# Kernel tuning notes

Hardware: AMD Instinct MI355X
Metric: run time of the kernel (lower is better)

## Reference

```python
import jax, jax.numpy as jnp
import numpy as np
from jax import lax

B, T, V = 128, 100, 100000
ED, MD, H = 300, 50, 512   # embed_dim, mask_dim, l_hidden_size
HH = H // 2                # per-direction GRU hidden
C1 = 0.1
C2 = 0.1


def _reverse_valid(x, lens):
    # reverse the valid prefix of each sequence (emulates packed-sequence reverse dir)
    t = jnp.arange(x.shape[1])[None, :]
    idx = jnp.where(t < lens[:, None], lens[:, None] - 1 - t, t)
    return jnp.take_along_axis(x, idx[:, :, None], axis=1)


def _gru_dir(x, valid, lens, wih, whh, bih, bhh, reverse):
    # x: [B,T,Din], valid: [B,T] bool. PyTorch GRU cell math, packed-seq semantics:
    # state frozen and output zeroed at padded steps.
    if reverse:
        x = _reverse_valid(x, lens)
    h0 = jnp.zeros((x.shape[0], whh.shape[1]), x.dtype)
    def step(h, inp):
        xt, mt = inp
        gi = xt @ wih.T + bih
        gh = h @ whh.T + bhh
        ir, iz, inn = jnp.split(gi, 3, axis=-1)
        hr, hz, hn = jnp.split(gh, 3, axis=-1)
        r = jax.nn.sigmoid(ir + hr)
        z = jax.nn.sigmoid(iz + hz)
        n = jnp.tanh(inn + r * hn)
        hnew = (1.0 - z) * n + z * h
        hnew = jnp.where(mt[:, None], hnew, h)
        return hnew, jnp.where(mt[:, None], hnew, 0.0)
    _, out = lax.scan(step, h0, (x.transpose(1, 0, 2), valid.T))
    out = out.transpose(1, 0, 2)
    if reverse:
        out = _reverse_valid(out, lens)
    return out


def _crf_marginals(feats, L, trans):
    # linear-chain CRF forward-backward marginals, 2 latent states; feats [T,2], valid length L
    Tm = feats.shape[0]
    def fstep(alpha, inp):
        ft, t = inp
        new = jax.nn.logsumexp(alpha[:, None] + trans, axis=0) + ft
        a = jnp.where(t < L, new, alpha)
        return a, a
    a0 = feats[0]
    _, rest = lax.scan(fstep, a0, (feats[1:], jnp.arange(1, Tm)))
    alphas = jnp.concatenate([a0[None], rest], axis=0)
    logZ = jax.nn.logsumexp(alphas[L - 1])
    def bstep(beta, inp):
        fn, t = inp
        cand = jax.nn.logsumexp(trans + (fn + beta)[None, :], axis=1)
        b = jnp.where(t >= L - 1, jnp.zeros_like(cand), cand)
        return b, b
    _, brev = lax.scan(bstep, jnp.zeros((2,), feats.dtype), (feats[1:][::-1], jnp.arange(Tm - 2, -1, -1)))
    betas = jnp.concatenate([brev[::-1], jnp.zeros((1, 2), feats.dtype)], axis=0)
    marg = jnp.exp(alphas + betas - logZ)
    return jnp.where(jnp.arange(Tm)[:, None] < L, marg, 0.0)


def setup_inputs():
    key = jax.random.key(0)
    ks = jax.random.split(key, 30)
    s = 0.08
    inp = {}
    inp["sents"] = jax.random.randint(ks[0], (B, T), 0, V, dtype=jnp.int32)
    lens = jnp.sort(jax.random.randint(ks[1], (B,), 5, T + 1, dtype=jnp.int32))[::-1]
    inp["lens"] = lens
    t = jnp.arange(T)[None, :]
    start = (lens // 3)[:, None]
    inp["masks"] = ((t >= start) & (t < start + 3)).astype(jnp.int32)
    inp["labels"] = jax.random.randint(ks[2], (B,), 0, 3, dtype=jnp.int32)
    inp["word_emb"] = jax.random.normal(ks[3], (V, ED)) * s
    inp["mask_emb"] = jax.random.normal(ks[4], (2, MD)) * s
    i = 5
    for l, din in ((0, ED + MD), (1, H)):
        for d in ("f", "b"):
            inp[f"gru{l}{d}_wih"] = jax.random.normal(ks[i], (3 * HH, din)) * s; i += 1
            inp[f"gru{l}{d}_whh"] = jax.random.normal(ks[i], (3 * HH, HH)) * s; i += 1
            inp[f"gru{l}{d}_bih"] = jnp.zeros((3 * HH,))
            inp[f"gru{l}{d}_bhh"] = jnp.zeros((3 * HH,))
    inp["conv_w"] = jax.random.normal(ks[i], (H, H, 3)) * s; i += 1
    inp["conv_b"] = jnp.zeros((H,))
    inp["tri_w"] = jax.random.normal(ks[i], (2, 2 * H)) * s; i += 1
    inp["tri_b"] = jnp.zeros((2,))
    inp["trans"] = jax.random.normal(ks[i], (2, 2)) * s; i += 1
    inp["lab_w"] = jax.random.normal(ks[i], (3, H)) * s; i += 1
    inp["lab_b"] = jnp.zeros((3,))
    return inp


def _forward(sents, masks, labels, lens, word_emb, mask_emb, gru_params, conv_w, conv_b, tri_w, tri_b, trans, lab_w, lab_b):
    x = jnp.concatenate([word_emb[sents], mask_emb[masks]], axis=-1)  # SimpleCat
    valid = jnp.arange(T)[None, :] < lens[:, None]
    for layer in range(2):  # 2-layer bidirectional GRU
        pf, pb = gru_params[2 * layer], gru_params[2 * layer + 1]
        f = _gru_dir(x, valid, lens, *pf, False)
        b = _gru_dir(x, valid, lens, *pb, True)
        x = jnp.concatenate([f, b], axis=-1)
    context = jax.nn.relu(
        lax.conv_general_dilated(x, conv_w.transpose(2, 1, 0), (1,), [(1, 1)],
                                 dimension_numbers=("NWC", "WIO", "NWC")) + conv_b)
    mf = masks.astype(context.dtype)
    avg = jnp.einsum("bt,bth->bh", mf, context) / mf.sum(1, keepdims=True)  # target avg emb
    ctx1 = jnp.concatenate([context, jnp.broadcast_to(avg[:, None, :], context.shape)], axis=-1)
    tri = ctx1 @ tri_w.T + tri_b  # [B,T,2]
    marg = jax.vmap(_crf_marginals, in_axes=(0, 0, None))(tri, lens, trans)
    sp = marg[:, :, 1]  # select polarity, zeroed beyond each sent_len
    sent_v = jnp.einsum("bt,bth->bh", sp, context)
    gamma = jnp.clip(sp.sum(1) / 2.0, 1e-4, 1e5)
    scores = (sent_v / gamma[:, None]) @ lab_w.T + lab_b
    logp = jax.nn.log_softmax(scores, axis=-1)
    cls_loss = -jnp.mean(jnp.take_along_axis(logp, labels[:, None], axis=1))  # NLLLoss
    s_norm = jnp.mean(sp.sum(1))  # mean L1 norm of nonneg marginals
    pena = jax.nn.relu(trans[1, 0] - trans[0, 0]) + jax.nn.relu(trans[0, 1] - trans[1, 1])
    return jnp.stack([cls_loss, C1 * pena + C2 * s_norm])


def reference(sents, masks, labels, lens, word_emb, mask_emb, gru0f_wih, gru0f_whh, gru0f_bih, gru0f_bhh, gru0b_wih, gru0b_whh, gru0b_bih, gru0b_bhh, gru1f_wih, gru1f_whh, gru1f_bih, gru1f_bhh, gru1b_wih, gru1b_whh, gru1b_bih, gru1b_bhh, conv_w, conv_b, tri_w, tri_b, trans, lab_w, lab_b):
    gp = ((gru0f_wih, gru0f_whh, gru0f_bih, gru0f_bhh),
          (gru0b_wih, gru0b_whh, gru0b_bih, gru0b_bhh),
          (gru1f_wih, gru1f_whh, gru1f_bih, gru1f_bhh),
          (gru1b_wih, gru1b_whh, gru1b_bih, gru1b_bhh))
    return _forward(sents, masks, labels, lens, word_emb, mask_emb, gp, conv_w, conv_b, tri_w, tri_b, trans, lab_w, lab_b)
```

## Files before the change

### kernel.cpp

```cpp
#include <hip/hip_runtime.h>
#include <hip/hip_bf16.h>
#include <stdint.h>


#define TT 100
#define BB 128

typedef short s16;
typedef unsigned int u32;
typedef __attribute__((ext_vector_type(8))) short s16x8;
typedef __attribute__((ext_vector_type(4))) float f32x4;
typedef __attribute__((ext_vector_type(2))) float f32x2;

__device__ __forceinline__ float bf2f(s16 s) {
  return __uint_as_float(((unsigned)(unsigned short)s) << 16);
}
__device__ __forceinline__ s16 f2bf(float f) {
  __hip_bfloat16 h = __float2bfloat16(f);
  return *(s16*)&h;
}
__device__ __forceinline__ float sigf(float x) { return 1.f / (1.f + __expf(-x)); }
__device__ __forceinline__ float tanhfast(float x) { return 2.f / (1.f + __expf(-2.f * x)) - 1.f; }
__device__ __forceinline__ float lse2(float a, float b) {
  float m = fmaxf(a, b);
  return m + logf(expf(a - m) + expf(b - m));
}


__global__ void k_cvtpad(const float* __restrict__ src, s16* __restrict__ dst) {
  int idx = blockIdx.x * 256 + threadIdx.x;
  if (idx >= 768 * 352) return;
  int n = idx / 352, k = idx % 352;
  dst[idx] = (k < 350) ? f2bf(src[n * 350 + k]) : (s16)0;
}

__global__ void k_cvt(const float* __restrict__ src, s16* __restrict__ dst, int n) {
  int idx = blockIdx.x * 256 + threadIdx.x;
  if (idx < n) dst[idx] = f2bf(src[idx]);
}

__global__ void k_wfrag(const float* __restrict__ whh, s16* __restrict__ wf) {
  int tid = blockIdx.x * 256 + threadIdx.x;
  if (tid >= 196608) return;
  int w = tid / 24576, rem = tid % 24576;
  int f = rem / 512, rem2 = rem % 512;
  int l = rem2 / 8, i = rem2 % 8;
  int nt = f / 8, kt = f % 8;
  int col = 96 * w + 16 * nt + (l & 15);
  int k = 32 * kt + 8 * (l >> 4) + i;
  wf[tid] = f2bf(whh[col * 256 + k]);
}

__global__ void k_w2(const float* __restrict__ cw, s16* __restrict__ w2) {
  int idx = blockIdx.x * 256 + threadIdx.x;
  if (idx >= 786432) return;
  int o = idx / 1536, c = idx % 1536;
  int w = c / 512, i = c % 512;
  w2[idx] = f2bf(cw[o * 1536 + i * 3 + w]);
}

__global__ void k_embed(const int* __restrict__ sents, const int* __restrict__ masks,
                        const float* __restrict__ wemb, const float* __restrict__ memb,
                        s16* __restrict__ x0) {
  int idx = blockIdx.x * 256 + threadIdx.x;
  if (idx >= BB * TT * 352) return;
  int c = idx % 352, bt = idx / 352;
  float v;
  if (c < 300)      v = wemb[(size_t)sents[bt] * 300 + c];
  else if (c < 350) v = memb[masks[bt] * 50 + (c - 300)];
  else              v = 0.f;
  x0[idx] = f2bf(v);
}

__global__ void k_zero16(uint4* __restrict__ p, int n16) {
  int idx = blockIdx.x * 256 + threadIdx.x;
  if (idx < n16) p[idx] = make_uint4(0u, 0u, 0u, 0u);
}

__global__ __launch_bounds__(256) void k_gemm(const s16* __restrict__ A, const s16* __restrict__ Bm,
                                              s16* __restrict__ C, int K, int ldA, int ldB, int ldC,
                                              const float* __restrict__ bias, int relu) {
  __shared__ s16 As[128 * 32];
  __shared__ s16 Bs[128 * 32];
  const int t = threadIdx.x, w = t >> 6, l = t & 63;
  const size_t m0 = (size_t)blockIdx.x * 128, n0 = (size_t)blockIdx.y * 128;
  f32x4 zero = {0.f, 0.f, 0.f, 0.f};
  f32x4 acc[4][4];
#pragma unroll
  for (int i = 0; i < 4; ++i)
#pragma unroll
    for (int j = 0; j < 4; ++j) acc[i][j] = zero;

  for (int kb = 0; kb < K; kb += 32) {
    __syncthreads();
    {
      const s16* gA = A + (m0 + (t >> 1)) * (size_t)ldA + kb + 16 * (t & 1);
      *(s16x8*)&As[(t >> 1) * 32 + 16 * (t & 1)]     = *(const s16x8*)gA;
      *(s16x8*)&As[(t >> 1) * 32 + 16 * (t & 1) + 8] = *(const s16x8*)(gA + 8);
      const s16* gB = Bm + (n0 + (t >> 1)) * (size_t)ldB + kb + 16 * (t & 1);
      *(s16x8*)&Bs[(t >> 1) * 32 + 16 * (t & 1)]     = *(const s16x8*)gB;
      *(s16x8*)&Bs[(t >> 1) * 32 + 16 * (t & 1) + 8] = *(const s16x8*)(gB + 8);
    }
    __syncthreads();
    s16x8 a[4], b[4];
#pragma unroll
    for (int i = 0; i < 4; ++i)
      a[i] = *(const s16x8*)&As[(64 * (w >> 1) + 16 * i + (l & 15)) * 32 + 8 * (l >> 4)];
#pragma unroll
    for (int j = 0; j < 4; ++j)
      b[j] = *(const s16x8*)&Bs[(64 * (w & 1) + 16 * j + (l & 15)) * 32 + 8 * (l >> 4)];
#pragma unroll
    for (int i = 0; i < 4; ++i)
#pragma unroll
      for (int j = 0; j < 4; ++j)
        acc[i][j] = __builtin_amdgcn_mfma_f32_16x16x32_bf16(a[i], b[j], acc[i][j], 0, 0, 0);
  }
#pragma unroll
  for (int i = 0; i < 4; ++i)
#pragma unroll
    for (int j = 0; j < 4; ++j)
#pragma unroll
      for (int r = 0; r < 4; ++r) {
        size_t row = m0 + 64 * (w >> 1) + 16 * i + 4 * (l >> 4) + r;
        size_t col = n0 + 64 * (w & 1) + 16 * j + (l & 15);
        float v = acc[i][j][r];
        if (bias) v += bias[col];
        if (relu) v = fmaxf(v, 0.f);
        C[row * (size_t)ldC + col] = f2bf(v);
      }
}

__global__ __launch_bounds__(512, 2) void k_gru(
    const s16* __restrict__ gi_f, const s16* __restrict__ gi_b,
    const s16* __restrict__ wf_f, const s16* __restrict__ wf_b,
    const float* __restrict__ bhh_f, const float* __restrict__ bhh_b,
    const int* __restrict__ lens, s16* __restrict__ out) {
  const int g = blockIdx.x;
  const int dir = blockIdx.y;
  const int tid = threadIdx.x, wid = tid >> 6, l = tid & 63;
  const s16* gi = dir ? gi_b : gi_f;
  const s16* wf = dir ? wf_b : wf_f;
  const float* bhh = dir ? bhh_b : bhh_f;
  const int col_off = dir ? 256 : 0;
  const int b0 = g * 8;

  __shared__ __align__(16) float gh2[16 * 772];
  __shared__ __align__(16) s16 hb[16 * 264];
  __shared__ float s_bhh[768];
  __shared__ int s_len[8];

  s16x8 wv[48];
#pragma unroll
  for (int f = 0; f < 48; ++f)
    wv[f] = *(const s16x8*)&wf[((size_t)(wid * 48 + f)) * 512 + l * 8];

  for (int i = tid; i < 16 * 264; i += 512) hb[i] = 0;
  for (int i = tid; i < 768; i += 512) s_bhh[i] = bhh[i];
  if (tid < 8) s_len[tid] = lens[b0 + tid];
  __syncthreads();

  const int smax = s_len[0];

  const int j0 = (tid & 127) * 2;
  const int r0 = tid >> 7;
  const int len0 = s_len[r0];
  const int len1 = s_len[r0 + 4];
  const float bhr0 = s_bhh[j0],       bhr1 = s_bhh[j0 + 1];
  const float bhz0 = s_bhh[256 + j0], bhz1 = s_bhh[257 + j0];
  const float bhn0 = s_bhh[512 + j0], bhn1 = s_bhh[513 + j0];
  float hp00 = 0.f, hp01 = 0.f, hp10 = 0.f, hp11 = 0.f;

  for (int s = 0; s < smax; ++s) {
    u32 q00 = 0, q01 = 0, q02 = 0, q10 = 0, q11 = 0, q12 = 0;
    int p0 = 0, p1 = 0;
    if (s < len0) {
      p0 = dir ? (len0 - 1 - s) : s;
      const s16* gp = gi + ((size_t)(b0 + r0) * TT + p0) * 768 + j0;
      q00 = *(const u32*)gp; q01 = *(const u32*)(gp + 256); q02 = *(const u32*)(gp + 512);
    }
    if (s < len1) {
      p1 = dir ? (len1 - 1 - s) : s;
      const s16* gp = gi + ((size_t)(b0 + r0 + 4) * TT + p1) * 768 + j0;
      q10 = *(const u32*)gp; q11 = *(const u32*)(gp + 256); q12 = *(const u32*)(gp + 512);
    }

    f32x4 zero = {0.f, 0.f, 0.f, 0.f};
    f32x4 acc[6];
#pragma unroll
    for (int nt = 0; nt < 6; ++nt) acc[nt] = zero;
#pragma unroll
    for (int kt = 0; kt < 8; ++kt) {
      s16x8 a = *(const s16x8*)&hb[(l & 15) * 264 + 32 * kt + 8 * (l >> 4)];
#pragma unroll
      for (int nt = 0; nt < 6; ++nt)
        acc[nt] = __builtin_amdgcn_mfma_f32_16x16x32_bf16(a, wv[nt * 8 + kt], acc[nt], 0, 0, 0);
    }
#pragma unroll
    for (int nt = 0; nt < 6; ++nt) {
      int col = 96 * wid + 16 * nt + (l & 15);
#pragma unroll
      for (int r = 0; r < 4; ++r)
        gh2[(4 * (l >> 4) + r) * 772 + col] = acc[nt][r];
    }
    __syncthreads();

    if (s < len0) {
      f32x2 gr = *(const f32x2*)&gh2[r0 * 772 + j0];
      f32x2 gz = *(const f32x2*)&gh2[r0 * 772 + 256 + j0];
      f32x2 gn = *(const f32x2*)&gh2[r0 * 772 + 512 + j0];
      float rr0 = sigf(bf2f((s16)(q00 & 0xffff)) + gr[0] + bhr0);
      float rr1 = sigf(bf2f((s16)(q00 >> 16))    + gr[1] + bhr1);
      float zz0 = sigf(bf2f((s16)(q01 & 0xffff)) + gz[0] + bhz0);
      float zz1 = sigf(bf2f((s16)(q01 >> 16))    + gz[1] + bhz1);
      float nn0 = tanhfast(bf2f((s16)(q02 & 0xffff)) + rr0 * (gn[0] + bhn0));
      float nn1 = tanhfast(bf2f((s16)(q02 >> 16))    + rr1 * (gn[1] + bhn1));
      hp00 = (1.f - zz0) * nn0 + zz0 * hp00;
      hp01 = (1.f - zz1) * nn1 + zz1 * hp01;
      u32 pk = (u32)(unsigned short)f2bf(hp00) | ((u32)(unsigned short)f2bf(hp01) << 16);
      *(u32*)&hb[r0 * 264 + j0] = pk;
      *(u32*)&out[((size_t)(b0 + r0) * TT + p0) * 512 + col_off + j0] = pk;
    }
    if (s < len1) {
      int row = r0 + 4;
      f32x2 gr = *(const f32x2*)&gh2[row * 772 + j0];
      f32x2 gz = *(const f32x2*)&gh2[row * 772 + 256 + j0];
      f32x2 gn = *(const f32x2*)&gh2[row * 772 + 512 + j0];
      float rr0 = sigf(bf2f((s16)(q10 & 0xffff)) + gr[0] + bhr0);
      float rr1 = sigf(bf2f((s16)(q10 >> 16))    + gr[1] + bhr1);
      float zz0 = sigf(bf2f((s16)(q11 & 0xffff)) + gz[0] + bhz0);
      float zz1 = sigf(bf2f((s16)(q11 >> 16))    + gz[1] + bhz1);
      float nn0 = tanhfast(bf2f((s16)(q12 & 0xffff)) + rr0 * (gn[0] + bhn0));
      float nn1 = tanhfast(bf2f((s16)(q12 >> 16))    + rr1 * (gn[1] + bhn1));
      hp10 = (1.f - zz0) * nn0 + zz0 * hp10;
      hp11 = (1.f - zz1) * nn1 + zz1 * hp11;
      u32 pk = (u32)(unsigned short)f2bf(hp10) | ((u32)(unsigned short)f2bf(hp11) << 16);
      *(u32*)&hb[row * 264 + j0] = pk;
      *(u32*)&out[((size_t)(b0 + row) * TT + p1) * 512 + col_off + j0] = pk;
    }
    __syncthreads();
  }
}

__global__ void k_im2col(const s16* __restrict__ x2, s16* __restrict__ A2) {
  int idx = blockIdx.x * 256 + threadIdx.x;
  if (idx >= 2457600) return;
  size_t e = (size_t)idx * 8;
  int bt = (int)(e / 1536), c = (int)(e % 1536);
  int w = c / 512, i = c % 512;
  int b = bt / TT, t = bt % TT;
  int ts = t + w - 1;
  s16x8 v;
  if (ts >= 0 && ts < TT) v = *(const s16x8*)&x2[(size_t)(b * TT + ts) * 512 + i];
  else { s16x8 z = {0,0,0,0,0,0,0,0}; v = z; }
  *(s16x8*)&A2[e] = v;
}

__global__ void k_avg(const s16* __restrict__ ctx, const int* __restrict__ masks,
                      float* __restrict__ avg) {
  int b = blockIdx.x, t = threadIdx.x;
  float a0 = 0, a1 = 0, ms = 0;
  for (int tt = 0; tt < TT; ++tt) {
    float mf = (float)masks[b * TT + tt];
    ms += mf;
    if (mf != 0.f) {
      a0 += mf * bf2f(ctx[(size_t)(b * TT + tt) * 512 + t]);
      a1 += mf * bf2f(ctx[(size_t)(b * TT + tt) * 512 + 256 + t]);
    }
  }
  avg[b * 512 + t] = a0 / ms;
  avg[b * 512 + 256 + t] = a1 / ms;
}

__global__ void k_tri(const s16* __restrict__ ctx, const float* __restrict__ avg,
                      const float* __restrict__ triw, const float* __restrict__ trib,
                      float* __restrict__ tri) {
  int gw = (blockIdx.x * 256 + threadIdx.x) >> 6;
  int l = threadIdx.x & 63;
  if (gw >= BB * TT) return;
  int b = gw / TT;
  float a0 = 0, a1 = 0;
  for (int it = 0; it < 16; ++it) {
    int k = l + 64 * it;
    float v = (k < 512) ? bf2f(ctx[(size_t)gw * 512 + k]) : avg[b * 512 + k - 512];
    a0 += v * triw[k];
    a1 += v * triw[1024 + k];
  }
  for (int off = 32; off; off >>= 1) {
    a0 += __shfl_down(a0, off, 64);
    a1 += __shfl_down(a1, off, 64);
  }
  if (l == 0) {
    tri[gw * 2]     = a0 + trib[0];
    tri[gw * 2 + 1] = a1 + trib[1];
  }
}

__global__ void k_crf(const float* __restrict__ tri, const int* __restrict__ lens,
                      const float* __restrict__ trans, float* __restrict__ alphas,
                      float* __restrict__ sp, float* __restrict__ sp_sum) {
  int b = threadIdx.x;
  int L = lens[b];
  float t00 = trans[0], t01 = trans[1], t10 = trans[2], t11 = trans[3];
  const float* f = tri + b * 2 * TT;
  float* al = alphas + b * 2 * TT;
  float a0 = f[0], a1 = f[1];
  al[0] = a0; al[1] = a1;
  for (int t = 1; t < TT; ++t) {
    if (t < L) {
      float n0 = lse2(a0 + t00, a1 + t10) + f[2 * t];
      float n1 = lse2(a0 + t01, a1 + t11) + f[2 * t + 1];
      a0 = n0; a1 = n1;
    }
    al[2 * t] = a0; al[2 * t + 1] = a1;
  }
  float logZ = lse2(a0, a1);
  float b0 = 0.f, b1 = 0.f, ssum = 0.f;
  {
    float v = (TT - 1 < L) ? expf(al[2 * (TT - 1) + 1] - logZ) : 0.f;
    sp[b * TT + TT - 1] = v; ssum += v;
  }
  for (int t = TT - 2; t >= 0; --t) {
    float fn0 = f[2 * (t + 1)], fn1 = f[2 * (t + 1) + 1];
    float c0 = lse2(t00 + fn0 + b0, t01 + fn1 + b1);
    float c1 = lse2(t10 + fn0 + b0, t11 + fn1 + b1);
    if (t >= L - 1) { b0 = 0.f; b1 = 0.f; } else { b0 = c0; b1 = c1; }
    float v = (t < L) ? expf(al[2 * t + 1] + b1 - logZ) : 0.f;
    sp[b * TT + t] = v; ssum += v;
  }
  sp_sum[b] = ssum;
}

__global__ void k_sentv(const s16* __restrict__ ctx, const float* __restrict__ sp,
                        float* __restrict__ sv) {
  int b = blockIdx.x, t = threadIdx.x;
  float a0 = 0, a1 = 0;
  for (int tt = 0; tt < TT; ++tt) {
    float w = sp[b * TT + tt];
    if (w != 0.f) {
      a0 += w * bf2f(ctx[(size_t)(b * TT + tt) * 512 + t]);
      a1 += w * bf2f(ctx[(size_t)(b * TT + tt) * 512 + 256 + t]);
    }
  }
  sv[b * 512 + t] = a0;
  sv[b * 512 + 256 + t] = a1;
}

__global__ void k_final(const float* __restrict__ sv, const float* __restrict__ sp_sum,
                        const int* __restrict__ labels, const float* __restrict__ labw,
                        const float* __restrict__ labb, const float* __restrict__ trans,
                        float* __restrict__ out) {
  __shared__ float red[128];
  int b = threadIdx.x;
  float g = sp_sum[b] * 0.5f;
  g = fminf(fmaxf(g, 1e-4f), 1e5f);
  float s[3];
  for (int c = 0; c < 3; ++c) {
    float a = 0.f;
    for (int h = 0; h < 512; ++h) a += sv[b * 512 + h] * labw[c * 512 + h];
    s[c] = a / g + labb[c];
  }
  float m = fmaxf(s[0], fmaxf(s[1], s[2]));
  float lse = m + logf(expf(s[0] - m) + expf(s[1] - m) + expf(s[2] - m));
  red[b] = -(s[labels[b]] - lse);
  __syncthreads();
  if (b == 0) {
    float acc = 0.f, sn = 0.f;
    for (int i = 0; i < 128; ++i) { acc += red[i]; sn += sp_sum[i]; }
    float pena = fmaxf(trans[2] - trans[0], 0.f) + fmaxf(trans[1] - trans[3], 0.f);
    out[0] = acc / 128.f;
    out[1] = 0.1f * pena + 0.1f * (sn / 128.f);
  }
}

extern "C" void kernel_launch(void* const* d_in, const int* in_sizes, int n_in,
                              void* d_out, int out_size, void* d_ws, size_t ws_size,
                              hipStream_t stream) {
  const int*   sents  = (const int*)d_in[0];
  const int*   lens   = (const int*)d_in[1];
  const int*   masks  = (const int*)d_in[2];
  const int*   labels = (const int*)d_in[3];
  const float* wemb   = (const float*)d_in[4];
  const float* memb   = (const float*)d_in[5];
  const float* wih0f = (const float*)d_in[6],  *whh0f = (const float*)d_in[7];
  const float* bih0f = (const float*)d_in[8],  *bhh0f = (const float*)d_in[9];
  const float* wih0b = (const float*)d_in[10], *whh0b = (const float*)d_in[11];
  const float* bih0b = (const float*)d_in[12], *bhh0b = (const float*)d_in[13];
  const float* wih1f = (const float*)d_in[14], *whh1f = (const float*)d_in[15];
  const float* bih1f = (const float*)d_in[16], *bhh1f = (const float*)d_in[17];
  const float* wih1b = (const float*)d_in[18], *whh1b = (const float*)d_in[19];
  const float* bih1b = (const float*)d_in[20], *bhh1b = (const float*)d_in[21];
  const float* convw = (const float*)d_in[22], *convb = (const float*)d_in[23];
  const float* triw  = (const float*)d_in[24], *trib  = (const float*)d_in[25];
  const float* trans = (const float*)d_in[26];
  const float* labw  = (const float*)d_in[27], *labb  = (const float*)d_in[28];
  float* out = (float*)d_out;
  char* ws = (char*)d_ws;

  s16* x0    = (s16*)(ws + 0);
  s16* cwih0f = (s16*)(ws + 9011200);
  s16* cwih0b = (s16*)(ws + 9551872);
  s16* cwih1f = (s16*)(ws + 10092544);
  s16* cwih1b = (s16*)(ws + 10878976);
  s16* wf0f  = (s16*)(ws + 11665408);
  s16* wf0b  = (s16*)(ws + 12058624);
  s16* wf1f  = (s16*)(ws + 12451840);
  s16* wf1b  = (s16*)(ws + 12845056);
  s16* w2    = (s16*)(ws + 13238272);
  s16* giF   = (s16*)(ws + 14811136);
  s16* giB   = (s16*)(ws + 34471936);
  s16* x1    = (s16*)(ws + 54132736);
  s16* x2    = (s16*)(ws + 67239936);
  s16* A2    = giF;
  s16* ctx   = x1;
  float* avg   = (float*)(ws + 80347136);
  float* tri   = (float*)(ws + 80609280);
  float* alphas= (float*)(ws + 80711680);
  float* sp    = (float*)(ws + 80814080);
  float* spsum = (float*)(ws + 80865280);
  float* sentv = (float*)(ws + 80865792);

  k_cvtpad<<<1056, 256, 0, stream>>>(wih0f, cwih0f);
  k_cvtpad<<<1056, 256, 0, stream>>>(wih0b, cwih0b);
  k_cvt<<<1536, 256, 0, stream>>>(wih1f, cwih1f, 393216);
  k_cvt<<<1536, 256, 0, stream>>>(wih1b, cwih1b, 393216);
  k_wfrag<<<768, 256, 0, stream>>>(whh0f, wf0f);
  k_wfrag<<<768, 256, 0, stream>>>(whh0b, wf0b);
  k_wfrag<<<768, 256, 0, stream>>>(whh1f, wf1f);
  k_wfrag<<<768, 256, 0, stream>>>(whh1b, wf1b);
  k_w2<<<3072, 256, 0, stream>>>(convw, w2);
  k_embed<<<17600, 256, 0, stream>>>(sents, masks, wemb, memb, x0);
  k_zero16<<<3200, 256, 0, stream>>>((uint4*)x1, 819200);
  k_zero16<<<3200, 256, 0, stream>>>((uint4*)x2, 819200);

  k_gemm<<<dim3(100, 6), 256, 0, stream>>>(x0, cwih0f, giF, 352, 352, 352, 768, bih0f, 0);
  k_gemm<<<dim3(100, 6), 256, 0, stream>>>(x0, cwih0b, giB, 352, 352, 352, 768, bih0b, 0);
  k_gru<<<dim3(16, 2), 512, 0, stream>>>(giF, giB, wf0f, wf0b, bhh0f, bhh0b, lens, x1);

  k_gemm<<<dim3(100, 6), 256, 0, stream>>>(x1, cwih1f, giF, 512, 512, 512, 768, bih1f, 0);
  k_gemm<<<dim3(100, 6), 256, 0, stream>>>(x1, cwih1b, giB, 512, 512, 512, 768, bih1b, 0);
  k_gru<<<dim3(16, 2), 512, 0, stream>>>(giF, giB, wf1f, wf1b, bhh1f, bhh1b, lens, x2);

  k_im2col<<<9600, 256, 0, stream>>>(x2, A2);
  k_gemm<<<dim3(100, 4), 256, 0, stream>>>(A2, w2, ctx, 1536, 1536, 1536, 512, convb, 1);
  k_avg<<<128, 256, 0, stream>>>(ctx, masks, avg);
  k_tri<<<3200, 256, 0, stream>>>(ctx, avg, triw, trib, tri);
  k_crf<<<1, 128, 0, stream>>>(tri, lens, trans, alphas, sp, spsum);
  k_sentv<<<128, 256, 0, stream>>>(ctx, sp, sentv);
  k_final<<<1, 128, 0, stream>>>(sentv, spsum, labels, labw, labb, trans, out);
}
```

Before: 1.143 ms.

## Split GRU across more blocks, prefetch gate inputs, fold bias, fuse prep kernels

The GRU recurrence now gives each block 4 batch rows instead of 8, doubling the block count so the sequential loop spreads across more CUs and each thread handles half the elementwise gate work. Next-step input-gate values are loaded one iteration ahead so the global-load latency overlaps the MFMA work. The hidden bias is used as the initial MFMA accumulator, which removes the shared-memory bias table. The twelve weight-conversion, embedding and zeroing launches are merged into one grid-stride kernel, and the zeroing of x1 is dropped. In exchange, MFMA tiles still cover 16 rows, so more of each tile computes on padding rows.

After: 1.010 ms. 1.13x faster.

```diff
diff --git a/kernel.cpp b/kernel.cpp
--- a/kernel.cpp
+++ b/kernel.cpp
@@ -26,55 +26,57 @@
   return m + logf(expf(a - m) + expf(b - m));
 }
 
-
-__global__ void k_cvtpad(const float* __restrict__ src, s16* __restrict__ dst) {
-  int idx = blockIdx.x * 256 + threadIdx.x;
-  if (idx >= 768 * 352) return;
-  int n = idx / 352, k = idx % 352;
-  dst[idx] = (k < 350) ? f2bf(src[n * 350 + k]) : (s16)0;
-}
-
-__global__ void k_cvt(const float* __restrict__ src, s16* __restrict__ dst, int n) {
-  int idx = blockIdx.x * 256 + threadIdx.x;
-  if (idx < n) dst[idx] = f2bf(src[idx]);
-}
-
-__global__ void k_wfrag(const float* __restrict__ whh, s16* __restrict__ wf) {
-  int tid = blockIdx.x * 256 + threadIdx.x;
-  if (tid >= 196608) return;
-  int w = tid / 24576, rem = tid % 24576;
-  int f = rem / 512, rem2 = rem % 512;
-  int l = rem2 / 8, i = rem2 % 8;
-  int nt = f / 8, kt = f % 8;
-  int col = 96 * w + 16 * nt + (l & 15);
-  int k = 32 * kt + 8 * (l >> 4) + i;
-  wf[tid] = f2bf(whh[col * 256 + k]);
-}
-
-__global__ void k_w2(const float* __restrict__ cw, s16* __restrict__ w2) {
-  int idx = blockIdx.x * 256 + threadIdx.x;
-  if (idx >= 786432) return;
-  int o = idx / 1536, c = idx % 1536;
-  int w = c / 512, i = c % 512;
-  w2[idx] = f2bf(cw[o * 1536 + i * 3 + w]);
-}
-
-__global__ void k_embed(const int* __restrict__ sents, const int* __restrict__ masks,
-                        const float* __restrict__ wemb, const float* __restrict__ memb,
-                        s16* __restrict__ x0) {
-  int idx = blockIdx.x * 256 + threadIdx.x;
-  if (idx >= BB * TT * 352) return;
-  int c = idx % 352, bt = idx / 352;
-  float v;
-  if (c < 300)      v = wemb[(size_t)sents[bt] * 300 + c];
-  else if (c < 350) v = memb[masks[bt] * 50 + (c - 300)];
-  else              v = 0.f;
-  x0[idx] = f2bf(v);
-}
-
-__global__ void k_zero16(uint4* __restrict__ p, int n16) {
-  int idx = blockIdx.x * 256 + threadIdx.x;
-  if (idx < n16) p[idx] = make_uint4(0u, 0u, 0u, 0u);
+__global__ void k_prep(const float* __restrict__ wih0f, const float* __restrict__ wih0b,
+                       const float* __restrict__ wih1f, const float* __restrict__ wih1b,
+                       const float* __restrict__ whh0f, const float* __restrict__ whh0b,
+                       const float* __restrict__ whh1f, const float* __restrict__ whh1b,
+                       const float* __restrict__ convw,
+                       const int* __restrict__ sents, const int* __restrict__ masks,
+                       const float* __restrict__ wemb, const float* __restrict__ memb,
+                       s16* __restrict__ cwih0f, s16* __restrict__ cwih0b,
+                       s16* __restrict__ cwih1f, s16* __restrict__ cwih1b,
+                       s16* __restrict__ wf0f, s16* __restrict__ wf0b,
+                       s16* __restrict__ wf1f, s16* __restrict__ wf1b,
+                       s16* __restrict__ w2, s16* __restrict__ x0,
+                       uint4* __restrict__ x2z) {
+  const int stride = gridDim.x * 256;
+  const int base = blockIdx.x * 256 + threadIdx.x;
+
+  for (int idx = base; idx < 768 * 352; idx += stride) {
+    int n = idx / 352, k = idx % 352;
+    cwih0f[idx] = (k < 350) ? f2bf(wih0f[n * 350 + k]) : (s16)0;
+    cwih0b[idx] = (k < 350) ? f2bf(wih0b[n * 350 + k]) : (s16)0;
+  }
+  for (int idx = base; idx < 393216; idx += stride) {
+    cwih1f[idx] = f2bf(wih1f[idx]);
+    cwih1b[idx] = f2bf(wih1b[idx]);
+  }
+  for (int idx = base; idx < 196608; idx += stride) {
+    int w = idx / 24576, rem = idx % 24576;
+    int f = rem / 512, rem2 = rem % 512;
+    int l = rem2 / 8, i = rem2 % 8;
+    int nt = f / 8, kt = f % 8;
+    int src = (96 * w + 16 * nt + (l & 15)) * 256 + 32 * kt + 8 * (l >> 4) + i;
+    wf0f[idx] = f2bf(whh0f[src]);
+    wf0b[idx] = f2bf(whh0b[src]);
+    wf1f[idx] = f2bf(whh1f[src]);
+    wf1b[idx] = f2bf(whh1b[src]);
+  }
+  for (int idx = base; idx < 786432; idx += stride) {
+    int o = idx / 1536, c = idx % 1536;
+    int w = c / 512, i = c % 512;
+    w2[idx] = f2bf(convw[o * 1536 + i * 3 + w]);
+  }
+  for (int idx = base; idx < BB * TT * 352; idx += stride) {
+    int c = idx % 352, bt = idx / 352;
+    float v;
+    if (c < 300)      v = wemb[(size_t)sents[bt] * 300 + c];
+    else if (c < 350) v = memb[masks[bt] * 50 + (c - 300)];
+    else              v = 0.f;
+    x0[idx] = f2bf(v);
+  }
+  for (int idx = base; idx < 819200; idx += stride)
+    x2z[idx] = make_uint4(0u, 0u, 0u, 0u);
 }
 
 __global__ __launch_bounds__(256) void k_gemm(const s16* __restrict__ A, const s16* __restrict__ Bm,
@@ -142,52 +144,52 @@
   const s16* wf = dir ? wf_b : wf_f;
   const float* bhh = dir ? bhh_b : bhh_f;
   const int col_off = dir ? 256 : 0;
-  const int b0 = g * 8;
+  const int b0 = g * 4;
 
   __shared__ __align__(16) float gh2[16 * 772];
   __shared__ __align__(16) s16 hb[16 * 264];
-  __shared__ float s_bhh[768];
-  __shared__ int s_len[8];
+  __shared__ int s_len[4];
 
   s16x8 wv[48];
 #pragma unroll
   for (int f = 0; f < 48; ++f)
     wv[f] = *(const s16x8*)&wf[((size_t)(wid * 48 + f)) * 512 + l * 8];
+  float bv[6];
+#pragma unroll
+  for (int nt = 0; nt < 6; ++nt) bv[nt] = bhh[96 * wid + 16 * nt + (l & 15)];
 
   for (int i = tid; i < 16 * 264; i += 512) hb[i] = 0;
-  for (int i = tid; i < 768; i += 512) s_bhh[i] = bhh[i];
-  if (tid < 8) s_len[tid] = lens[b0 + tid];
+  if (tid < 4) s_len[tid] = lens[b0 + tid];
   __syncthreads();
 
   const int smax = s_len[0];
-
+  const int row = tid >> 7;
   const int j0 = (tid & 127) * 2;
-  const int r0 = tid >> 7;
-  const int len0 = s_len[r0];
-  const int len1 = s_len[r0 + 4];
-  const float bhr0 = s_bhh[j0],       bhr1 = s_bhh[j0 + 1];
-  const float bhz0 = s_bhh[256 + j0], bhz1 = s_bhh[257 + j0];
-  const float bhn0 = s_bhh[512 + j0], bhn1 = s_bhh[513 + j0];
-  float hp00 = 0.f, hp01 = 0.f, hp10 = 0.f, hp11 = 0.f;
+  const int len = s_len[row];
+  const s16* gbase = gi + (size_t)(b0 + row) * TT * 768 + j0;
+  s16* obase = out + (size_t)(b0 + row) * TT * 512 + col_off + j0;
+  float hp0 = 0.f, hp1 = 0.f;
+
+  u32 qa0, qa1, qa2;
+  int pa;
+  {
+    pa = dir ? (len - 1) : 0;
+    const s16* gp = gbase + (size_t)pa * 768;
+    qa0 = *(const u32*)gp; qa1 = *(const u32*)(gp + 256); qa2 = *(const u32*)(gp + 512);
+  }
 
   for (int s = 0; s < smax; ++s) {
-    u32 q00 = 0, q01 = 0, q02 = 0, q10 = 0, q11 = 0, q12 = 0;
-    int p0 = 0, p1 = 0;
-    if (s < len0) {
-      p0 = dir ? (len0 - 1 - s) : s;
-      const s16* gp = gi + ((size_t)(b0 + r0) * TT + p0) * 768 + j0;
-      q00 = *(const u32*)gp; q01 = *(const u32*)(gp + 256); q02 = *(const u32*)(gp + 512);
-    }
-    if (s < len1) {
-      p1 = dir ? (len1 - 1 - s) : s;
-      const s16* gp = gi + ((size_t)(b0 + r0 + 4) * TT + p1) * 768 + j0;
-      q10 = *(const u32*)gp; q11 = *(const u32*)(gp + 256); q12 = *(const u32*)(gp + 512);
-    }
-
-    f32x4 zero = {0.f, 0.f, 0.f, 0.f};
+    u32 qb0 = 0, qb1 = 0, qb2 = 0;
+    int pb = 0;
+    if (s + 1 < len) {
+      pb = dir ? (len - 2 - s) : (s + 1);
+      const s16* gp = gbase + (size_t)pb * 768;
+      qb0 = *(const u32*)gp; qb1 = *(const u32*)(gp + 256); qb2 = *(const u32*)(gp + 512);
+    }
+
     f32x4 acc[6];
 #pragma unroll
-    for (int nt = 0; nt < 6; ++nt) acc[nt] = zero;
+    for (int nt = 0; nt < 6; ++nt) { f32x4 b = {bv[nt], bv[nt], bv[nt], bv[nt]}; acc[nt] = b; }
 #pragma unroll
     for (int kt = 0; kt < 8; ++kt) {
       s16x8 a = *(const s16x8*)&hb[(l & 15) * 264 + 32 * kt + 8 * (l >> 4)];
@@ -204,40 +206,24 @@
     }
     __syncthreads();
 
-    if (s < len0) {
-      f32x2 gr = *(const f32x2*)&gh2[r0 * 772 + j0];
-      f32x2 gz = *(const f32x2*)&gh2[r0 * 772 + 256 + j0];
-      f32x2 gn = *(const f32x2*)&gh2[r0 * 772 + 512 + j0];
-      float rr0 = sigf(bf2f((s16)(q00 & 0xffff)) + gr[0] + bhr0);
-      float rr1 = sigf(bf2f((s16)(q00 >> 16))    + gr[1] + bhr1);
-      float zz0 = sigf(bf2f((s16)(q01 & 0xffff)) + gz[0] + bhz0);
-      float zz1 = sigf(bf2f((s16)(q01 >> 16))    + gz[1] + bhz1);
-      float nn0 = tanhfast(bf2f((s16)(q02 & 0xffff)) + rr0 * (gn[0] + bhn0));
-      float nn1 = tanhfast(bf2f((s16)(q02 >> 16))    + rr1 * (gn[1] + bhn1));
-      hp00 = (1.f - zz0) * nn0 + zz0 * hp00;
-      hp01 = (1.f - zz1) * nn1 + zz1 * hp01;
-      u32 pk = (u32)(unsigned short)f2bf(hp00) | ((u32)(unsigned short)f2bf(hp01) << 16);
-      *(u32*)&hb[r0 * 264 + j0] = pk;
-      *(u32*)&out[((size_t)(b0 + r0) * TT + p0) * 512 + col_off + j0] = pk;
-    }
-    if (s < len1) {
-      int row = r0 + 4;
+    if (s < len) {
       f32x2 gr = *(const f32x2*)&gh2[row * 772 + j0];
       f32x2 gz = *(const f32x2*)&gh2[row * 772 + 256 + j0];
       f32x2 gn = *(const f32x2*)&gh2[row * 772 + 512 + j0];
-      float rr0 = sigf(bf2f((s16)(q10 & 0xffff)) + gr[0] + bhr0);
-      float rr1 = sigf(bf2f((s16)(q10 >> 16))    + gr[1] + bhr1);
-      float zz0 = sigf(bf2f((s16)(q11 & 0xffff)) + gz[0] + bhz0);
-      float zz1 = sigf(bf2f((s16)(q11 >> 16))    + gz[1] + bhz1);
-      float nn0 = tanhfast(bf2f((s16)(q12 & 0xffff)) + rr0 * (gn[0] + bhn0));
-      float nn1 = tanhfast(bf2f((s16)(q12 >> 16))    + rr1 * (gn[1] + bhn1));
-      hp10 = (1.f - zz0) * nn0 + zz0 * hp10;
-      hp11 = (1.f - zz1) * nn1 + zz1 * hp11;
-      u32 pk = (u32)(unsigned short)f2bf(hp10) | ((u32)(unsigned short)f2bf(hp11) << 16);
+      float rr0 = sigf(bf2f((s16)(qa0 & 0xffff)) + gr[0]);
+      float rr1 = sigf(bf2f((s16)(qa0 >> 16))    + gr[1]);
+      float zz0 = sigf(bf2f((s16)(qa1 & 0xffff)) + gz[0]);
+      float zz1 = sigf(bf2f((s16)(qa1 >> 16))    + gz[1]);
+      float nn0 = tanhfast(bf2f((s16)(qa2 & 0xffff)) + rr0 * gn[0]);
+      float nn1 = tanhfast(bf2f((s16)(qa2 >> 16))    + rr1 * gn[1]);
+      hp0 = (1.f - zz0) * nn0 + zz0 * hp0;
+      hp1 = (1.f - zz1) * nn1 + zz1 * hp1;
+      u32 pk = (u32)(unsigned short)f2bf(hp0) | ((u32)(unsigned short)f2bf(hp1) << 16);
       *(u32*)&hb[row * 264 + j0] = pk;
-      *(u32*)&out[((size_t)(b0 + row) * TT + p1) * 512 + col_off + j0] = pk;
+      *(u32*)&obase[(size_t)pa * 512] = pk;
     }
     __syncthreads();
+    qa0 = qb0; qa1 = qb1; qa2 = qb2; pa = pb;
   }
 }
 
@@ -419,26 +405,19 @@
   float* spsum = (float*)(ws + 80865280);
   float* sentv = (float*)(ws + 80865792);
 
-  k_cvtpad<<<1056, 256, 0, stream>>>(wih0f, cwih0f);
-  k_cvtpad<<<1056, 256, 0, stream>>>(wih0b, cwih0b);
-  k_cvt<<<1536, 256, 0, stream>>>(wih1f, cwih1f, 393216);
-  k_cvt<<<1536, 256, 0, stream>>>(wih1b, cwih1b, 393216);
-  k_wfrag<<<768, 256, 0, stream>>>(whh0f, wf0f);
-  k_wfrag<<<768, 256, 0, stream>>>(whh0b, wf0b);
-  k_wfrag<<<768, 256, 0, stream>>>(whh1f, wf1f);
-  k_wfrag<<<768, 256, 0, stream>>>(whh1b, wf1b);
-  k_w2<<<3072, 256, 0, stream>>>(convw, w2);
-  k_embed<<<17600, 256, 0, stream>>>(sents, masks, wemb, memb, x0);
-  k_zero16<<<3200, 256, 0, stream>>>((uint4*)x1, 819200);
-  k_zero16<<<3200, 256, 0, stream>>>((uint4*)x2, 819200);
+  k_prep<<<2048, 256, 0, stream>>>(wih0f, wih0b, wih1f, wih1b,
+                                   whh0f, whh0b, whh1f, whh1b, convw,
+                                   sents, masks, wemb, memb,
+                                   cwih0f, cwih0b, cwih1f, cwih1b,
+                                   wf0f, wf0b, wf1f, wf1b, w2, x0, (uint4*)x2);
 
   k_gemm<<<dim3(100, 6), 256, 0, stream>>>(x0, cwih0f, giF, 352, 352, 352, 768, bih0f, 0);
   k_gemm<<<dim3(100, 6), 256, 0, stream>>>(x0, cwih0b, giB, 352, 352, 352, 768, bih0b, 0);
-  k_gru<<<dim3(16, 2), 512, 0, stream>>>(giF, giB, wf0f, wf0b, bhh0f, bhh0b, lens, x1);
+  k_gru<<<dim3(32, 2), 512, 0, stream>>>(giF, giB, wf0f, wf0b, bhh0f, bhh0b, lens, x1);
 
   k_gemm<<<dim3(100, 6), 256, 0, stream>>>(x1, cwih1f, giF, 512, 512, 512, 768, bih1f, 0);
   k_gemm<<<dim3(100, 6), 256, 0, stream>>>(x1, cwih1b, giB, 512, 512, 512, 768, bih1b, 0);
-  k_gru<<<dim3(16, 2), 512, 0, stream>>>(giF, giB, wf1f, wf1b, bhh1f, bhh1b, lens, x2);
+  k_gru<<<dim3(32, 2), 512, 0, stream>>>(giF, giB, wf1f, wf1b, bhh1f, bhh1b, lens, x2);
 
   k_im2col<<<9600, 256, 0, stream>>>(x2, A2);
   k_gemm<<<dim3(100, 4), 256, 0, stream>>>(A2, w2, ctx, 1536, 1536, 1536, 512, convb, 1);
```
